# Kernel tuning notes

Measured on AMD Instinct MI355X. Metric: run time of the kernel, lower is better.

## Reference

```python
import jax, jax.numpy as jnp
import numpy as np

N_NODES = 10000
N_EDGES = 160000
N_GRAPHS = 16
IN_FEAT = 128
DIMS = [(128, 512), (512, 256), (256, 64), (64, 32)]


def _lin_params(key, fin, fout):
    w = jax.random.normal(key, (fin, fout), jnp.float32) * (1.0 / np.sqrt(fin))
    b = jnp.zeros((fout,), jnp.float32)
    return w, b


def setup_inputs() -> dict:
    key = jax.random.key(0)
    ks = jax.random.split(key, 64)
    inp = {}
    inp['x'] = jax.random.normal(ks[0], (N_NODES, IN_FEAT), jnp.float32)
    inp['edge_index'] = jax.random.randint(ks[1], (2, N_EDGES), 0, N_NODES, jnp.int64 if jax.config.jax_enable_x64 else jnp.int32)
    inp['batch'] = jnp.sort(jax.random.randint(ks[2], (N_NODES,), 0, N_GRAPHS))
    ki = 3
    for li, (fin, fout) in enumerate(DIMS, start=1):
        for nm in ['q', 'k', 'v', 's']:
            w, b = _lin_params(ks[ki], fin, fout); ki += 1
            inp[f'W{nm}{li}'] = w
            inp[f'b{nm}{li}'] = b
    inp['Wg'], inp['bg'] = _lin_params(ks[ki], 32, 1); ki += 1
    inp['Wf'], inp['bf'] = _lin_params(ks[ki], 32, 9)
    return inp


def _segment_softmax(logits, seg, num_segments):
    m = jax.ops.segment_max(logits, seg, num_segments=num_segments)
    e = jnp.exp(logits - m[seg])
    s = jax.ops.segment_sum(e, seg, num_segments=num_segments)
    return e / s[seg]


def _transformer_conv(x, src, dst, Wq, bq, Wk, bk, Wv, bv, Ws, bs):
    # PyG TransformerConv, heads=1: attention over incoming edges per dst node.
    n = x.shape[0]
    q = x @ Wq + bq
    k = x @ Wk + bk
    v = x @ Wv + bv
    d = q.shape[-1]
    logits = jnp.sum(q[dst] * k[src], axis=-1) / jnp.sqrt(jnp.asarray(d, x.dtype))
    alpha = _segment_softmax(logits, dst, n)  # [E]
    agg = jax.ops.segment_sum(alpha[:, None] * v[src], dst, num_segments=n)
    return agg + (x @ Ws + bs)  # root/skip connection


def reference(x, edge_index, batch,
              Wq1, bq1, Wk1, bk1, Wv1, bv1, Ws1, bs1,
              Wq2, bq2, Wk2, bk2, Wv2, bv2, Ws2, bs2,
              Wq3, bq3, Wk3, bk3, Wv3, bv3, Ws3, bs3,
              Wq4, bq4, Wk4, bk4, Wv4, bv4, Ws4, bs4,
              Wg, bg, Wf, bf):
    src, dst = edge_index[0], edge_index[1]
    layers = [
        (Wq1, bq1, Wk1, bk1, Wv1, bv1, Ws1, bs1),
        (Wq2, bq2, Wk2, bk2, Wv2, bv2, Ws2, bs2),
        (Wq3, bq3, Wk3, bk3, Wv3, bv3, Ws3, bs3),
        (Wq4, bq4, Wk4, bk4, Wv4, bv4, Ws4, bs4),
    ]
    h = x
    for p in layers:
        h = jax.nn.elu(_transformer_conv(h, src, dst, *p))
    # GlobalAttention pooling: gate softmax per graph, weighted sum.
    gate = (h @ Wg + bg)[:, 0]  # [N]
    a = _segment_softmax(gate, batch, N_GRAPHS)
    pooled = jax.ops.segment_sum(a[:, None] * h, batch, num_segments=N_GRAPHS)  # [G, 32]
    return pooled @ Wf + bf  # [G, 9]
```

## Files before the change

### kernel.cpp

```cpp
#include <hip/hip_runtime.h>
#include <hip/hip_bf16.h>
#include <math.h>


typedef __bf16 bf16x8 __attribute__((ext_vector_type(8)));
typedef __bf16 bf16x4 __attribute__((ext_vector_type(4)));
typedef __bf16 bf16x2 __attribute__((ext_vector_type(2)));
typedef float f32x4 __attribute__((ext_vector_type(4)));
typedef float f32x2 __attribute__((ext_vector_type(2)));

#define GBM 128
#define GBN 128
#define GBK 64

#if __has_builtin(__builtin_amdgcn_global_load_lds)
#define ASYNC_LDS 1
__device__ __forceinline__ void gload16(const __bf16* g, __bf16* l) {
  __builtin_amdgcn_global_load_lds(
      (const __attribute__((address_space(1))) unsigned int*)g,
      (__attribute__((address_space(3))) unsigned int*)l, 16, 0, 0);
}
#endif

#if __has_builtin(__builtin_amdgcn_fdot2_f32_bf16)
#define HAS_BF16_DOT2 1
#endif

__global__ __launch_bounds__(256) void gemm_mfma_kernel(
    const __bf16* __restrict__ A, const __bf16* __restrict__ Bt,
    const float* __restrict__ bias, __bf16* __restrict__ qkvs,
    int M, int K, int Nc) {
  __shared__ __bf16 As[GBM * 64];
  __shared__ __bf16 Bs[GBN * 64];
  const int tid = threadIdx.x;
  const int wave = tid >> 6;
  const int lane = tid & 63;
  const int quad = lane >> 4;
  const int l16 = lane & 15;
  const int m0 = blockIdx.y * GBM;
  const int n0 = blockIdx.x * GBN;
  const int wm = (wave & 1) * 64;
  const int wn = (wave >> 1) * 64;

  const int r8 = lane >> 3;
  const int sseg = lane & 7;

  f32x4 acc[4][4] = {};

  for (int k0 = 0; k0 < K; k0 += GBK) {
#pragma unroll
    for (int it = 0; it < 4; ++it) {
      const int rbase = wave * 32 + it * 8;
      const int row = rbase + r8;
      const int sw = sseg ^ r8;
      const __bf16* ga = A + (size_t)(m0 + row) * K + k0 + sw * 8;
      const __bf16* gb = Bt + (size_t)(n0 + row) * K + k0 + sw * 8;
#ifdef ASYNC_LDS
      gload16(ga, As + rbase * 64);
      gload16(gb, Bs + rbase * 64);
#else
      *(bf16x8*)(As + row * 64 + sseg * 8) = *(const bf16x8*)ga;
      *(bf16x8*)(Bs + row * 64 + sseg * 8) = *(const bf16x8*)gb;
#endif
    }
    __syncthreads();

#pragma unroll
    for (int ks = 0; ks < 2; ++ks) {
      bf16x8 af[4], bfr[4];
#pragma unroll
      for (int i = 0; i < 4; ++i) {
        const int ra = wm + i * 16 + l16;
        const int rb = wn + i * 16 + l16;
        const int ps = ((ks * 4 + quad) ^ (l16 & 7)) * 8;
        af[i]  = *(const bf16x8*)(As + ra * 64 + ps);
        bfr[i] = *(const bf16x8*)(Bs + rb * 64 + ps);
      }
#pragma unroll
      for (int mi = 0; mi < 4; ++mi)
#pragma unroll
        for (int ni = 0; ni < 4; ++ni)
          acc[mi][ni] = __builtin_amdgcn_mfma_f32_16x16x32_bf16(
              af[mi], bfr[ni], acc[mi][ni], 0, 0, 0);
    }
    __syncthreads();
  }

  float bsv[4];
#pragma unroll
  for (int ni = 0; ni < 4; ++ni) bsv[ni] = bias[n0 + wn + ni * 16 + l16];
#pragma unroll
  for (int mi = 0; mi < 4; ++mi) {
#pragma unroll
    for (int r = 0; r < 4; ++r) {
      int row = m0 + wm + mi * 16 + quad * 4 + r;
      if (row < M) {
        size_t rb = (size_t)row * Nc;
#pragma unroll
        for (int ni = 0; ni < 4; ++ni) {
          int col = n0 + wn + ni * 16 + l16;
          qkvs[rb + col] = (__bf16)(acc[mi][ni][r] + bsv[ni]);
        }
      }
    }
  }
}

__global__ __launch_bounds__(256) void gemm_mfma_elu_kernel(
    const __bf16* __restrict__ A, const __bf16* __restrict__ Bt,
    const float* __restrict__ bias_s, const float* __restrict__ bias_v,
    const int* __restrict__ offs, __bf16* __restrict__ out,
    int M, int K, int Nc) {
  __shared__ __bf16 As[GBM * 64];
  __shared__ __bf16 Bs[GBN * 64];
  const int tid = threadIdx.x;
  const int wave = tid >> 6;
  const int lane = tid & 63;
  const int quad = lane >> 4;
  const int l16 = lane & 15;
  const int m0 = blockIdx.y * GBM;
  const int n0 = blockIdx.x * GBN;
  const int wm = (wave & 1) * 64;
  const int wn = (wave >> 1) * 64;

  const int r8 = lane >> 3;
  const int sseg = lane & 7;

  f32x4 acc[4][4] = {};

  for (int k0 = 0; k0 < K; k0 += GBK) {
#pragma unroll
    for (int it = 0; it < 4; ++it) {
      const int rbase = wave * 32 + it * 8;
      const int row = rbase + r8;
      const int sw = sseg ^ r8;
      const __bf16* ga = A + (size_t)(m0 + row) * K + k0 + sw * 8;
      const __bf16* gb = Bt + (size_t)(n0 + row) * K + k0 + sw * 8;
#ifdef ASYNC_LDS
      gload16(ga, As + rbase * 64);
      gload16(gb, Bs + rbase * 64);
#else
      *(bf16x8*)(As + row * 64 + sseg * 8) = *(const bf16x8*)ga;
      *(bf16x8*)(Bs + row * 64 + sseg * 8) = *(const bf16x8*)gb;
#endif
    }
    __syncthreads();

#pragma unroll
    for (int ks = 0; ks < 2; ++ks) {
      bf16x8 af[4], bfr[4];
#pragma unroll
      for (int i = 0; i < 4; ++i) {
        const int ra = wm + i * 16 + l16;
        const int rb = wn + i * 16 + l16;
        const int ps = ((ks * 4 + quad) ^ (l16 & 7)) * 8;
        af[i]  = *(const bf16x8*)(As + ra * 64 + ps);
        bfr[i] = *(const bf16x8*)(Bs + rb * 64 + ps);
      }
#pragma unroll
      for (int mi = 0; mi < 4; ++mi)
#pragma unroll
        for (int ni = 0; ni < 4; ++ni)
          acc[mi][ni] = __builtin_amdgcn_mfma_f32_16x16x32_bf16(
              af[mi], bfr[ni], acc[mi][ni], 0, 0, 0);
    }
    __syncthreads();
  }

  float bsv[4], bvv[4];
#pragma unroll
  for (int ni = 0; ni < 4; ++ni) {
    const int col = n0 + wn + ni * 16 + l16;
    bsv[ni] = bias_s[col];
    bvv[ni] = bias_v[col];
  }
#pragma unroll
  for (int mi = 0; mi < 4; ++mi) {
#pragma unroll
    for (int r = 0; r < 4; ++r) {
      int row = m0 + wm + mi * 16 + quad * 4 + r;
      if (row < M) {
        const float bm = (offs[row + 1] - offs[row]) > 0 ? 1.f : 0.f;
        size_t rb = (size_t)row * Nc;
#pragma unroll
        for (int ni = 0; ni < 4; ++ni) {
          int col = n0 + wn + ni * 16 + l16;
          float v = acc[mi][ni][r] + bsv[ni] + bm * bvv[ni];
          v = (v > 0.f) ? v : expm1f(v);
          out[rb + col] = (__bf16)v;
        }
      }
    }
  }
}

#define NTILES 180
__global__ __launch_bounds__(256) void transpose_w_kernel(
    const float* W1q, const float* W1k, const float* W1v, const float* W1s,
    const float* W2q, const float* W2k, const float* W2v, const float* W2s,
    const float* W3q, const float* W3k, const float* W3v, const float* W3s,
    const float* W0v, const float* W0s,
    __bf16* __restrict__ Wt, __bf16* __restrict__ Bt2) {
  __shared__ float tile[64][65];
  const int tb = blockIdx.x;
  const int tid = threadIdx.x;

  const float* src;
  __bf16* dst;
  int K, F, RS, CO, k0, j0;
  if (tb < 128) {
    const int m = tb >> 5, t = tb & 31;
    const float* Ws[4] = {W1q, W1k, W1v, W1s};
    src = Ws[m]; K = 512; F = 256; RS = 512; CO = 0;
    k0 = (t & 7) * 64; j0 = (t >> 3) * 64;
    dst = Wt + 262144 + (size_t)m * 131072;
  } else if (tb < 144) {
    const int u = tb - 128, m = u >> 2;
    const float* Ws[4] = {W2q, W2k, W2v, W2s};
    src = Ws[m]; K = 256; F = 64; RS = 256; CO = 0;
    k0 = (u & 3) * 64; j0 = 0;
    dst = Wt + 786432 + (size_t)m * 16384;
  } else if (tb < 148) {
    const int m = tb - 144;
    const float* Ws[4] = {W3q, W3k, W3v, W3s};
    src = Ws[m]; K = 64; F = 32; RS = 64; CO = 0;
    k0 = 0; j0 = 0;
    dst = Wt + 851968 + (size_t)m * 2048;
  } else {
    const int u = tb - 148, m = u >> 4, t = u & 15;
    src = m ? W0s : W0v; K = 128; F = 512; RS = 256; CO = m * 128;
    k0 = (t & 1) * 64; j0 = (t >> 1) * 64;
    dst = Bt2;
  }

  const int lj = tid & 63;
  const int lr = tid >> 6;
#pragma unroll
  for (int it = 0; it < 16; ++it) {
    const int kr = it * 4 + lr;
    float v = 0.f;
    if (k0 + kr < K && j0 + lj < F) v = src[(size_t)(k0 + kr) * F + j0 + lj];
    tile[kr][lj] = v;
  }
  __syncthreads();
#pragma unroll
  for (int it = 0; it < 16; ++it) {
    const int jr = it * 4 + lr;
    if (j0 + jr < F && k0 + lj < K)
      dst[(size_t)(j0 + jr) * RS + CO + k0 + lj] = (__bf16)tile[lj][jr];
  }
}

#define BTOT 3456
#define XTOT 320000
#define ABT_T 65536
#define UB_T 512
__global__ void pack_misc_kernel(
    const float* b0q, const float* b0k, const float* b0v, const float* b0s,
    const float* b1q, const float* b1k, const float* b1v, const float* b1s,
    const float* b2q, const float* b2k, const float* b2v, const float* b2s,
    const float* b3q, const float* b3k, const float* b3v, const float* b3s,
    const float* W0q, const float* W0k,
    const float* __restrict__ x, __bf16* __restrict__ xb,
    float* __restrict__ bcat,
    const int* __restrict__ dst, int* __restrict__ deg, int E,
    __bf16* __restrict__ Abt, float* __restrict__ biasu) {
  const int t = blockIdx.x * 256 + threadIdx.x;
  if (t < XTOT) {
    float4 v = ((const float4*)x)[t];
    bf16x4 o;
    o[0] = (__bf16)v.x; o[1] = (__bf16)v.y; o[2] = (__bf16)v.z; o[3] = (__bf16)v.w;
    *(bf16x4*)(xb + (size_t)t * 4) = o;
  } else if (t < XTOT + BTOT) {
    int u = t - XTOT;
    int l, local, fsh, boff;
    if (u < 2048)      { l = 0; local = u;        fsh = 9; boff = 0; }
    else if (u < 3072) { l = 1; local = u - 2048; fsh = 8; boff = 2048; }
    else if (u < 3328) { l = 2; local = u - 3072; fsh = 6; boff = 3072; }
    else               { l = 3; local = u - 3328; fsh = 5; boff = 3328; }
    const int fout = 1 << fsh;
    int blk = local >> fsh, j = local & (fout - 1);
    const float* b;
    if (l == 0)      b = blk == 0 ? b0q : blk == 1 ? b0k : blk == 2 ? b0v : b0s;
    else if (l == 1) b = blk == 0 ? b1q : blk == 1 ? b1k : blk == 2 ? b1v : b1s;
    else if (l == 2) b = blk == 0 ? b2q : blk == 1 ? b2k : blk == 2 ? b2v : b2s;
    else             b = blk == 0 ? b3q : blk == 1 ? b3k : blk == 2 ? b3v : b3s;
    bcat[boff + local] = b[j];
  } else if (t < XTOT + BTOT + E) {
    int e = t - (XTOT + BTOT);
    atomicAdd(&deg[dst[e]], 1);
  } else if (t < XTOT + BTOT + E + ABT_T) {
    const int u = t - (XTOT + BTOT + E);
    const int n = u >> 9;
    const int rem = u & 511;
    const int k = rem >> 2;
    const int q = rem & 3;
    const float4* wq = (const float4*)(W0q + (size_t)k * 512) + q * 32;
    const float4* wk = (const float4*)(W0k + (size_t)n * 512) + q * 32;
    float sacc = 0.f;
#pragma unroll 4
    for (int jj = 0; jj < 32; ++jj) {
      float4 a = wq[jj], b = wk[jj];
      sacc += a.x * b.x + a.y * b.y + a.z * b.z + a.w * b.w;
    }
    sacc += __shfl_xor(sacc, 1);
    sacc += __shfl_xor(sacc, 2);
    if (q == 0) Abt[(size_t)n * 128 + k] = (__bf16)sacc;
  } else if (t < XTOT + BTOT + E + ABT_T + UB_T) {
    const int u = t - (XTOT + BTOT + E + ABT_T);
    const int n = u >> 2;
    const int q = u & 3;
    const float4* wk = (const float4*)(W0k + (size_t)n * 512) + q * 32;
    const float4* bq = (const float4*)b0q + q * 32;
    float sacc = 0.f;
#pragma unroll 4
    for (int jj = 0; jj < 32; ++jj) {
      float4 a = wk[jj], b = bq[jj];
      sacc += a.x * b.x + a.y * b.y + a.z * b.z + a.w * b.w;
    }
    sacc += __shfl_xor(sacc, 1);
    sacc += __shfl_xor(sacc, 2);
    if (q == 0) biasu[n] = sacc;
  }
}

__global__ __launch_bounds__(1024) void scan_kernel(const int* __restrict__ deg,
                                                    int* __restrict__ offs, int N) {
  __shared__ int sums[1024];
  const int tid = threadIdx.x;
  const int chunk = (N + 1023) / 1024;
  const int start = tid * chunk;
  int s = 0;
  for (int i = 0; i < chunk; ++i) {
    int idx = start + i;
    if (idx < N) s += deg[idx];
  }
  sums[tid] = s;
  __syncthreads();
  for (int off = 1; off < 1024; off <<= 1) {
    int t = (tid >= off) ? sums[tid - off] : 0;
    __syncthreads();
    sums[tid] += t;
    __syncthreads();
  }
  int run = (tid == 0) ? 0 : sums[tid - 1];
  for (int i = 0; i < chunk; ++i) {
    int idx = start + i;
    if (idx < N) {
      offs[idx] = run;
      run += deg[idx];
    }
  }
  if (tid == 1023) offs[N] = sums[1023];
}

__global__ void scatter_kernel(const int* __restrict__ src, const int* __restrict__ dst,
                               const int* __restrict__ offs, int* __restrict__ cursor,
                               int* __restrict__ csr_src, int E) {
  int e = blockIdx.x * blockDim.x + threadIdx.x;
  if (e >= E) return;
  int d = dst[e];
  int pos = offs[d] + atomicAdd(&cursor[d], 1);
  csr_src[pos] = src[e];
}

template <int D, int LPG_LOG2, bool GATE>
__global__ __launch_bounds__(256) void attn_fused_kernel(
    const __bf16* __restrict__ qkvs, const int* __restrict__ csr_src,
    const int* __restrict__ offs, __bf16* __restrict__ h_out, int N,
    float scale, const float* __restrict__ Wg, const float* __restrict__ bg,
    float* __restrict__ gate_out) {
  constexpr int LPG = 1 << LPG_LOG2;
  constexpr int NG = 64 / LPG;
  constexpr int NIT = D / (8 * LPG);
  constexpr int LD = 4 * D;
  const int node = (blockIdx.x * 256 + threadIdx.x) >> 6;
  const int lane = threadIdx.x & 63;
  if (node >= N) return;
  const int g = lane >> LPG_LOG2;
  const int l = lane & (LPG - 1);
  const int begin = offs[node];
  const int deg = offs[node + 1] - begin;

  const __bf16* qrow = qkvs + (size_t)node * LD;
  bf16x8 qreg[NIT];
#pragma unroll
  for (int it = 0; it < NIT; ++it)
    qreg[it] = *(const bf16x8*)(qrow + it * LPG * 8 + l * 8);

  float m0 = 0.f;
  float s = 0.f;
  f32x2 acc[NIT][4] = {};

  bf16x8 kA[NIT], vA[NIT], kB[NIT], vB[NIT];

  auto load_rows = [&](bool valid, int idx, bf16x8 (&kv)[NIT], bf16x8 (&vv)[NIT]) {
    const int sidx = valid ? csr_src[begin + idx] : 0;
    const __bf16* kr = qkvs + (size_t)sidx * LD + D + l * 8;
    if (valid) {
#pragma unroll
      for (int it = 0; it < NIT; ++it) {
        kv[it] = *(const bf16x8*)(kr + it * LPG * 8);
        vv[it] = *(const bf16x8*)(kr + D + it * LPG * 8);
      }
    }
  };

  auto compute = [&](bool valid, bool first, const bf16x8 (&kv)[NIT],
                     const bf16x8 (&vv)[NIT]) {
    float p = 0.f;
    if (valid) {
#ifdef HAS_BF16_DOT2
#pragma unroll
      for (int it = 0; it < NIT; ++it)
#pragma unroll
        for (int j2 = 0; j2 < 4; ++j2) {
          bf16x2 qa; qa[0] = qreg[it][2 * j2]; qa[1] = qreg[it][2 * j2 + 1];
          bf16x2 ka; ka[0] = kv[it][2 * j2];   ka[1] = kv[it][2 * j2 + 1];
          p = __builtin_amdgcn_fdot2_f32_bf16(qa, ka, p, false);
        }
#else
#pragma unroll
      for (int it = 0; it < NIT; ++it)
#pragma unroll
        for (int j = 0; j < 8; ++j) p += (float)qreg[it][j] * (float)kv[it][j];
#endif
    }
#pragma unroll
    for (int off = LPG >> 1; off; off >>= 1) p += __shfl_xor(p, off);
    const float logit = valid ? p * scale : -INFINITY;

    if (first) {
      float mm = logit;
#pragma unroll
      for (int off = LPG; off < 64; off <<= 1)
        mm = fmaxf(mm, __shfl_xor(mm, off));
      m0 = mm;
    }

    const float w = __expf(logit - m0);
    s += w;
    if (valid) {
      f32x2 w2; w2[0] = w; w2[1] = w;
#pragma unroll
      for (int it = 0; it < NIT; ++it)
#pragma unroll
        for (int j2 = 0; j2 < 4; ++j2) {
          f32x2 vf;
          vf[0] = (float)vv[it][2 * j2];
          vf[1] = (float)vv[it][2 * j2 + 1];
          acc[it][j2] += w2 * vf;
        }
    }
  };

  bool valA = g < deg;
  load_rows(valA, g, kA, vA);
  for (int base = 0; base < deg; base += 2 * NG) {
    const bool valB = base + NG + g < deg;
    load_rows(valB, base + NG + g, kB, vB);
    compute(valA, base == 0, kA, vA);
    valA = base + 2 * NG + g < deg;
    load_rows(valA, base + 2 * NG + g, kA, vA);
    compute(valB, false, kB, vB);
  }

#pragma unroll
  for (int off = LPG; off < 64; off <<= 1) {
    s += __shfl_xor(s, off);
#pragma unroll
    for (int it = 0; it < NIT; ++it)
#pragma unroll
      for (int j2 = 0; j2 < 4; ++j2) {
        acc[it][j2][0] += __shfl_xor(acc[it][j2][0], off);
        acc[it][j2][1] += __shfl_xor(acc[it][j2][1], off);
      }
  }
  const float inv = (deg > 0) ? (1.0f / s) : 0.f;

  if (g == 0) {
    float rr[NIT][8];
#pragma unroll
    for (int it = 0; it < NIT; ++it) {
      const int f0 = it * LPG * 8 + l * 8;
      bf16x8 sk = *(const bf16x8*)(qrow + 3 * D + f0);
      bf16x8 o;
#pragma unroll
      for (int j2 = 0; j2 < 4; ++j2) {
        float r0 = acc[it][j2][0] * inv + (float)sk[2 * j2];
        float r1 = acc[it][j2][1] * inv + (float)sk[2 * j2 + 1];
        r0 = (r0 > 0.f) ? r0 : expm1f(r0);
        r1 = (r1 > 0.f) ? r1 : expm1f(r1);
        rr[it][2 * j2] = r0;
        rr[it][2 * j2 + 1] = r1;
        o[2 * j2] = (__bf16)r0;
        o[2 * j2 + 1] = (__bf16)r1;
      }
      *(bf16x8*)(h_out + (size_t)node * D + f0) = o;
    }
    if (GATE) {
      float gp = 0.f;
#pragma unroll
      for (int j = 0; j < 8; ++j) gp += rr[0][j] * Wg[l * 8 + j];
#pragma unroll
      for (int off = 1; off < LPG; off <<= 1) gp += __shfl_xor(gp, off);
      if (l == 0) gate_out[node] = gp + bg[0];
    }
  }
}

template <int LPG_LOG2>
__global__ __launch_bounds__(256) void attn_lin_kernel(
    const __bf16* __restrict__ u, const __bf16* __restrict__ hsrc,
    const int* __restrict__ csr_src, const int* __restrict__ offs,
    __bf16* __restrict__ buf, int N, float scale) {
  constexpr int D = 128;
  constexpr int LPG = 1 << LPG_LOG2;
  constexpr int NG = 64 / LPG;
  constexpr int NIT = D / (8 * LPG);
  const int node = (blockIdx.x * 256 + threadIdx.x) >> 6;
  const int lane = threadIdx.x & 63;
  if (node >= N) return;
  const int g = lane >> LPG_LOG2;
  const int l = lane & (LPG - 1);
  const int begin = offs[node];
  const int deg = offs[node + 1] - begin;

  const __bf16* urow = u + (size_t)node * D;
  bf16x8 qreg[NIT];
#pragma unroll
  for (int it = 0; it < NIT; ++it)
    qreg[it] = *(const bf16x8*)(urow + it * LPG * 8 + l * 8);

  float m0 = 0.f;
  float s = 0.f;
  f32x2 acc[NIT][4] = {};

  bf16x8 kA[NIT], kB[NIT];

  auto load_rows = [&](bool valid, int idx, bf16x8 (&kv)[NIT]) {
    const int sidx = valid ? csr_src[begin + idx] : 0;
    const __bf16* hr = hsrc + (size_t)sidx * D + l * 8;
    if (valid) {
#pragma unroll
      for (int it = 0; it < NIT; ++it)
        kv[it] = *(const bf16x8*)(hr + it * LPG * 8);
    }
  };

  auto compute = [&](bool valid, bool first, const bf16x8 (&kv)[NIT]) {
    float p = 0.f;
    if (valid) {
#ifdef HAS_BF16_DOT2
#pragma unroll
      for (int it = 0; it < NIT; ++it)
#pragma unroll
        for (int j2 = 0; j2 < 4; ++j2) {
          bf16x2 qa; qa[0] = qreg[it][2 * j2]; qa[1] = qreg[it][2 * j2 + 1];
          bf16x2 ka; ka[0] = kv[it][2 * j2];   ka[1] = kv[it][2 * j2 + 1];
          p = __builtin_amdgcn_fdot2_f32_bf16(qa, ka, p, false);
        }
#else
#pragma unroll
      for (int it = 0; it < NIT; ++it)
#pragma unroll
        for (int j = 0; j < 8; ++j) p += (float)qreg[it][j] * (float)kv[it][j];
#endif
    }
#pragma unroll
    for (int off = LPG >> 1; off; off >>= 1) p += __shfl_xor(p, off);
    const float logit = valid ? p * scale : -INFINITY;

    if (first) {
      float mm = logit;
#pragma unroll
      for (int off = LPG; off < 64; off <<= 1)
        mm = fmaxf(mm, __shfl_xor(mm, off));
      m0 = mm;
    }

    const float w = __expf(logit - m0);
    s += w;
    if (valid) {
      f32x2 w2; w2[0] = w; w2[1] = w;
#pragma unroll
      for (int it = 0; it < NIT; ++it)
#pragma unroll
        for (int j2 = 0; j2 < 4; ++j2) {
          f32x2 vf;
          vf[0] = (float)kv[it][2 * j2];
          vf[1] = (float)kv[it][2 * j2 + 1];
          acc[it][j2] += w2 * vf;
        }
    }
  };

  bool valA = g < deg;
  load_rows(valA, g, kA);
  for (int base = 0; base < deg; base += 2 * NG) {
    const bool valB = base + NG + g < deg;
    load_rows(valB, base + NG + g, kB);
    compute(valA, base == 0, kA);
    valA = base + 2 * NG + g < deg;
    load_rows(valA, base + 2 * NG + g, kA);
    compute(valB, false, kB);
  }

#pragma unroll
  for (int off = LPG; off < 64; off <<= 1) {
    s += __shfl_xor(s, off);
#pragma unroll
    for (int it = 0; it < NIT; ++it)
#pragma unroll
      for (int j2 = 0; j2 < 4; ++j2) {
        acc[it][j2][0] += __shfl_xor(acc[it][j2][0], off);
        acc[it][j2][1] += __shfl_xor(acc[it][j2][1], off);
      }
  }
  const float inv = (deg > 0) ? (1.0f / s) : 0.f;

  if (g == 0) {
#pragma unroll
    for (int it = 0; it < NIT; ++it) {
      const int f0 = it * LPG * 8 + l * 8;
      bf16x8 o;
#pragma unroll
      for (int j2 = 0; j2 < 4; ++j2) {
        o[2 * j2]     = (__bf16)(acc[it][j2][0] * inv);
        o[2 * j2 + 1] = (__bf16)(acc[it][j2][1] * inv);
      }
      *(bf16x8*)(buf + (size_t)node * 256 + f0) = o;
      *(bf16x8*)(buf + (size_t)node * 256 + 128 + f0) =
          *(const bf16x8*)(hsrc + (size_t)node * D + f0);
    }
  }
}

__global__ __launch_bounds__(256) void pool_final_kernel(
    const __bf16* __restrict__ h, const float* __restrict__ gate,
    const int* __restrict__ batch, int N, const float* __restrict__ Wf,
    const float* __restrict__ bf_, float* __restrict__ out) {
  __shared__ float red[256];
  __shared__ float pooled_s[32];
  __shared__ float m_s, inv_s;
  __shared__ int sb[2];
  const int g = blockIdx.x;
  const int tid = threadIdx.x;

  if (tid < 2) {
    int target = g + tid;
    int lo = 0, hi = N;
    while (lo < hi) {
      int mid = (lo + hi) >> 1;
      if (batch[mid] < target) lo = mid + 1;
      else hi = mid;
    }
    sb[tid] = lo;
  }
  __syncthreads();
  const int s = sb[0];
  const int e_end = sb[1];

  float m = -INFINITY;
  for (int i = s + tid; i < e_end; i += 256) m = fmaxf(m, gate[i]);
  red[tid] = m;
  __syncthreads();
  for (int off = 128; off; off >>= 1) {
    if (tid < off) red[tid] = fmaxf(red[tid], red[tid + off]);
    __syncthreads();
  }
  if (tid == 0) m_s = red[0];
  __syncthreads();
  m = m_s;

  float ss = 0.f;
  for (int i = s + tid; i < e_end; i += 256) ss += __expf(gate[i] - m);
  red[tid] = ss;
  __syncthreads();
  for (int off = 128; off; off >>= 1) {
    if (tid < off) red[tid] += red[tid + off];
    __syncthreads();
  }
  if (tid == 0) inv_s = (e_end > s) ? (1.0f / red[0]) : 0.f;
  __syncthreads();
  const float inv = inv_s;

  const int f = tid & 31;
  const int grp = tid >> 5;
  float acc = 0.f;
  for (int i = s + grp; i < e_end; i += 8)
    acc += __expf(gate[i] - m) * (float)h[(size_t)i * 32 + f];
  red[tid] = acc;
  __syncthreads();
  if (tid < 32) {
    float a = 0.f;
#pragma unroll
    for (int j = 0; j < 8; ++j) a += red[j * 32 + tid];
    pooled_s[tid] = a * inv;
  }
  __syncthreads();

  if (tid < 9) {
    float o = bf_[tid];
#pragma unroll
    for (int kk = 0; kk < 32; ++kk) o += pooled_s[kk] * Wf[kk * 9 + tid];
    out[g * 9 + tid] = o;
  }
}

#define WTOT 860160
#define ATOT 16384
#define UBTOT 128
#define B2TOT 131072
extern "C" void kernel_launch(void* const* d_in, const int* in_sizes, int n_in,
                              void* d_out, int out_size, void* d_ws, size_t ws_size,
                              hipStream_t stream) {
  const int N = in_sizes[2];
  const int E = in_sizes[1] / 2;
  const int G = 16;
  const int NP = N + 128;

  const float* x = (const float*)d_in[0];
  const int* ei = (const int*)d_in[1];
  const int* batch = (const int*)d_in[2];
  const int* src = ei;
  const int* dst = ei + E;
  const float* Wg = (const float*)d_in[35];
  const float* bg = (const float*)d_in[36];
  const float* Wf = (const float*)d_in[37];
  const float* bf_ = (const float*)d_in[38];
  float* out = (float*)d_out;

  char* p = (char*)d_ws;
  auto carve = [&](size_t bytes) -> char* {
    char* r = p;
    p += (bytes + 255) & ~(size_t)255;
    return r;
  };
  int* deg = (int*)carve((size_t)2 * N * 4);
  int* cursor = deg + N;
  int* offs = (int*)carve((size_t)(N + 1) * 4);
  int* csr_src = (int*)carve((size_t)E * 4);
  __bf16* Ab = (__bf16*)carve((size_t)NP * 128 * 2);
  __bf16* Wt = (__bf16*)carve((size_t)WTOT * 2);
  float* bcat = (float*)carve(BTOT * 4);
  __bf16* qkvs = (__bf16*)carve((size_t)NP * 1024 * 2);
  __bf16* ha = (__bf16*)carve((size_t)NP * 512 * 2);
  __bf16* hb = (__bf16*)carve((size_t)NP * 512 * 2);
  float* gate = (float*)carve((size_t)N * 4);
  __bf16* ubuf = (__bf16*)carve((size_t)NP * 128 * 2);
  __bf16* cat = (__bf16*)carve((size_t)NP * 256 * 2);
  __bf16* Abt = (__bf16*)carve((size_t)ATOT * 2);
  float* biasu = (float*)carve((size_t)UBTOT * 4);
  __bf16* Bt2 = (__bf16*)carve((size_t)B2TOT * 2);
  (void)ws_size;

  hipMemsetAsync(deg, 0, (size_t)2 * N * 4, stream);
  const float** di = (const float**)d_in;
  transpose_w_kernel<<<NTILES, 256, 0, stream>>>(
      di[11], di[13], di[15], di[17],
      di[19], di[21], di[23], di[25],
      di[27], di[29], di[31], di[33],
      di[7], di[9],
      Wt, Bt2);
  pack_misc_kernel<<<(XTOT + BTOT + E + ABT_T + UB_T + 255) / 256, 256, 0, stream>>>(
      di[4], di[6], di[8], di[10],
      di[12], di[14], di[16], di[18],
      di[20], di[22], di[24], di[26],
      di[28], di[30], di[32], di[34],
      di[3], di[5],
      x, Ab, bcat, dst, deg, E, Abt, biasu);
  scan_kernel<<<1, 1024, 0, stream>>>(deg, offs, N);
  scatter_kernel<<<(E + 255) / 256, 256, 0, stream>>>(src, dst, offs, cursor, csr_src, E);

  const int agrid = ((size_t)N * 64 + 255) / 256;
  const int mg = (N + GBM - 1) / GBM;

  {
    dim3 g1(1, mg);
    gemm_mfma_kernel<<<g1, 256, 0, stream>>>(Ab, Abt, biasu, ubuf, N, 128, 128);
    attn_lin_kernel<3><<<agrid, 256, 0, stream>>>(ubuf, Ab, csr_src, offs, cat, N,
                                                  1.0f / sqrtf(512.f));
    dim3 g2(4, mg);
    gemm_mfma_elu_kernel<<<g2, 256, 0, stream>>>(cat, Bt2, di[10], di[8], offs,
                                                 ha, N, 256, 512);
  }

  const int fins[3] = {512, 256, 64};
  const int fouts[3] = {256, 64, 32};
  const size_t woffs[3] = {262144, 786432, 851968};
  const int boffs[3] = {2048, 3072, 3328};
  const __bf16* hin = ha;
  __bf16* houts[3] = {hb, ha, hb};

  for (int l = 0; l < 3; ++l) {
    const int fin = fins[l], fout = fouts[l];
    const int Nc = 4 * fout;
    __bf16* hout = houts[l];

    dim3 grid(Nc / GBN, mg);
    gemm_mfma_kernel<<<grid, 256, 0, stream>>>(hin, Wt + woffs[l], bcat + boffs[l],
                                               qkvs, N, fin, Nc);

    float scale = 1.0f / sqrtf((float)fout);
    if (l == 0) {
      attn_fused_kernel<256, 4, false><<<agrid, 256, 0, stream>>>(
          qkvs, csr_src, offs, hout, N, scale, nullptr, nullptr, nullptr);
    } else if (l == 1) {
      attn_fused_kernel<64, 3, false><<<agrid, 256, 0, stream>>>(
          qkvs, csr_src, offs, hout, N, scale, nullptr, nullptr, nullptr);
    } else {
      attn_fused_kernel<32, 2, true><<<agrid, 256, 0, stream>>>(
          qkvs, csr_src, offs, hout, N, scale, Wg, bg, gate);
    }
    hin = hout;
  }

  pool_final_kernel<<<G, 256, 0, stream>>>(hin, gate, batch, N, Wf, bf_, out);
}
```

Baseline: 336.2 us.

## Split preprocessing kernel, tile Wq·Wkᵀ product through LDS, add XCD block swizzle

The monolithic preprocessing kernel is split into separate kernels: an edge-degree histogram, the x cast with bias packing, and a dedicated kernel that computes the layer-1 Wq·Wkᵀ matrix. The new kernel stages Wq rows and a Wk row in shared memory instead of having each thread stream 512-float rows from global memory. The two MFMA GEMM kernels also remap block indices so that consecutive tiles land on the same XCD, which is meant to improve L2 locality. The cost is extra kernel launches and a 1-in-4 active-thread compute phase in the new kernel.

```diff
diff --git a/kernel.cpp b/kernel.cpp
--- a/kernel.cpp
+++ b/kernel.cpp
@@ -25,6 +25,17 @@
 #if __has_builtin(__builtin_amdgcn_fdot2_f32_bf16)
 #define HAS_BF16_DOT2 1
 #endif
+
+__device__ __forceinline__ void xcd_swizzle(int& bx, int& by) {
+  const int gx = gridDim.x;
+  const int nwg = gx * gridDim.y;
+  const int orig = blockIdx.y * gx + blockIdx.x;
+  const int q = nwg >> 3, r = nwg & 7;
+  const int xcd = orig & 7, ii = orig >> 3;
+  const int wgid = (xcd < r ? xcd * (q + 1) : r * (q + 1) + (xcd - r) * q) + ii;
+  bx = wgid % gx;
+  by = wgid / gx;
+}
 
 __global__ __launch_bounds__(256) void gemm_mfma_kernel(
     const __bf16* __restrict__ A, const __bf16* __restrict__ Bt,
@@ -37,8 +48,10 @@
   const int lane = tid & 63;
   const int quad = lane >> 4;
   const int l16 = lane & 15;
-  const int m0 = blockIdx.y * GBM;
-  const int n0 = blockIdx.x * GBN;
+  int bx, by;
+  xcd_swizzle(bx, by);
+  const int m0 = by * GBM;
+  const int n0 = bx * GBN;
   const int wm = (wave & 1) * 64;
   const int wn = (wave >> 1) * 64;
 
@@ -118,8 +131,10 @@
   const int lane = tid & 63;
   const int quad = lane >> 4;
   const int l16 = lane & 15;
-  const int m0 = blockIdx.y * GBM;
-  const int n0 = blockIdx.x * GBN;
+  int bx, by;
+  xcd_swizzle(bx, by);
+  const int m0 = by * GBM;
+  const int n0 = bx * GBN;
   const int wm = (wave & 1) * 64;
   const int wn = (wave >> 1) * 64;
 
@@ -251,20 +266,23 @@
   }
 }
 
+__global__ void hist_kernel(const int* __restrict__ dst, int* __restrict__ deg,
+                            int E) {
+  const int e = blockIdx.x * 256 + threadIdx.x;
+  if (e < E) atomicAdd(&deg[dst[e]], 1);
+}
+
 #define BTOT 3456
 #define XTOT 320000
-#define ABT_T 65536
 #define UB_T 512
-__global__ void pack_misc_kernel(
+__global__ void xcast_misc_kernel(
     const float* b0q, const float* b0k, const float* b0v, const float* b0s,
     const float* b1q, const float* b1k, const float* b1v, const float* b1s,
     const float* b2q, const float* b2k, const float* b2v, const float* b2s,
     const float* b3q, const float* b3k, const float* b3v, const float* b3s,
-    const float* W0q, const float* W0k,
+    const float* W0k,
     const float* __restrict__ x, __bf16* __restrict__ xb,
-    float* __restrict__ bcat,
-    const int* __restrict__ dst, int* __restrict__ deg, int E,
-    __bf16* __restrict__ Abt, float* __restrict__ biasu) {
+    float* __restrict__ bcat, float* __restrict__ biasu) {
   const int t = blockIdx.x * 256 + threadIdx.x;
   if (t < XTOT) {
     float4 v = ((const float4*)x)[t];
@@ -286,28 +304,8 @@
     else if (l == 2) b = blk == 0 ? b2q : blk == 1 ? b2k : blk == 2 ? b2v : b2s;
     else             b = blk == 0 ? b3q : blk == 1 ? b3k : blk == 2 ? b3v : b3s;
     bcat[boff + local] = b[j];
-  } else if (t < XTOT + BTOT + E) {
-    int e = t - (XTOT + BTOT);
-    atomicAdd(&deg[dst[e]], 1);
-  } else if (t < XTOT + BTOT + E + ABT_T) {
-    const int u = t - (XTOT + BTOT + E);
-    const int n = u >> 9;
-    const int rem = u & 511;
-    const int k = rem >> 2;
-    const int q = rem & 3;
-    const float4* wq = (const float4*)(W0q + (size_t)k * 512) + q * 32;
-    const float4* wk = (const float4*)(W0k + (size_t)n * 512) + q * 32;
-    float sacc = 0.f;
-#pragma unroll 4
-    for (int jj = 0; jj < 32; ++jj) {
-      float4 a = wq[jj], b = wk[jj];
-      sacc += a.x * b.x + a.y * b.y + a.z * b.z + a.w * b.w;
-    }
-    sacc += __shfl_xor(sacc, 1);
-    sacc += __shfl_xor(sacc, 2);
-    if (q == 0) Abt[(size_t)n * 128 + k] = (__bf16)sacc;
-  } else if (t < XTOT + BTOT + E + ABT_T + UB_T) {
-    const int u = t - (XTOT + BTOT + E + ABT_T);
+  } else if (t < XTOT + BTOT + UB_T) {
+    const int u = t - (XTOT + BTOT);
     const int n = u >> 2;
     const int q = u & 3;
     const float4* wk = (const float4*)(W0k + (size_t)n * 512) + q * 32;
@@ -322,6 +320,53 @@
     sacc += __shfl_xor(sacc, 2);
     if (q == 0) biasu[n] = sacc;
   }
+}
+
+__global__ __launch_bounds__(256) void abt_kernel(
+    const float* __restrict__ W0q, const float* __restrict__ W0k,
+    __bf16* __restrict__ Abt) {
+  __shared__ float chq[64][132];
+  __shared__ float chk[128];
+  const int tid = threadIdx.x;
+  const int n = blockIdx.x >> 1;
+  const int k0 = (blockIdx.x & 1) * 64;
+  const int q = tid & 3;
+  const int kloc = tid >> 2;
+
+  float sacc = 0.f;
+#pragma unroll
+  for (int pass = 0; pass < 4; ++pass) {
+    {
+      const int c4 = (tid & 31) * 4;
+#pragma unroll
+      for (int it = 0; it < 8; ++it) {
+        const int row = it * 8 + (tid >> 5);
+        const float4 v = *(const float4*)(W0q + (size_t)(k0 + row) * 512 +
+                                          pass * 128 + c4);
+        chq[row][c4] = v.x; chq[row][c4 + 1] = v.y;
+        chq[row][c4 + 2] = v.z; chq[row][c4 + 3] = v.w;
+      }
+      if (tid < 32) {
+        const float4 v = *(const float4*)(W0k + (size_t)n * 512 +
+                                          pass * 128 + tid * 4);
+        chk[tid * 4] = v.x; chk[tid * 4 + 1] = v.y;
+        chk[tid * 4 + 2] = v.z; chk[tid * 4 + 3] = v.w;
+      }
+    }
+    __syncthreads();
+    if (q == pass) {
+#pragma unroll 4
+      for (int jj = 0; jj < 32; ++jj) {
+        float4 a = *(const float4*)&chq[kloc][jj * 4];
+        float4 b = *(const float4*)&chk[jj * 4];
+        sacc += a.x * b.x + a.y * b.y + a.z * b.z + a.w * b.w;
+      }
+    }
+    __syncthreads();
+  }
+  sacc += __shfl_xor(sacc, 1);
+  sacc += __shfl_xor(sacc, 2);
+  if (q == 0) Abt[(size_t)n * 128 + k0 + kloc] = (__bf16)sacc;
 }
 
 __global__ __launch_bounds__(1024) void scan_kernel(const int* __restrict__ deg,
@@ -757,19 +802,21 @@
 
   hipMemsetAsync(deg, 0, (size_t)2 * N * 4, stream);
   const float** di = (const float**)d_in;
+  hist_kernel<<<(E + 255) / 256, 256, 0, stream>>>(dst, deg, E);
   transpose_w_kernel<<<NTILES, 256, 0, stream>>>(
       di[11], di[13], di[15], di[17],
       di[19], di[21], di[23], di[25],
       di[27], di[29], di[31], di[33],
       di[7], di[9],
       Wt, Bt2);
-  pack_misc_kernel<<<(XTOT + BTOT + E + ABT_T + UB_T + 255) / 256, 256, 0, stream>>>(
+  xcast_misc_kernel<<<(XTOT + BTOT + UB_T + 255) / 256, 256, 0, stream>>>(
       di[4], di[6], di[8], di[10],
       di[12], di[14], di[16], di[18],
       di[20], di[22], di[24], di[26],
       di[28], di[30], di[32], di[34],
-      di[3], di[5],
-      x, Ab, bcat, dst, deg, E, Abt, biasu);
+      di[5],
+      x, Ab, bcat, biasu);
+  abt_kernel<<<256, 256, 0, stream>>>(di[3], di[5], Abt);
   scan_kernel<<<1, 1024, 0, stream>>>(deg, offs, N);
   scatter_kernel<<<(E + 255) / 256, 256, 0, stream>>>(src, dst, offs, cursor, csr_src, E);
 
```

Measured after the change: 335.7 us. Within noise of the previous version (-0.2%).
